# Kernel optimization log

Measured on AMD Instinct MI355X. Metric: run time of the kernel, lower is better.

## Reference

```python
import jax, jax.numpy as jnp
import numpy as np

B, T, F, U = 64, 512, 1024, 64


def setup_inputs() -> dict:
    key = jax.random.key(0)
    ks = jax.random.split(key, 6)
    return {
        "x": jax.random.normal(ks[0], (B, T, F), dtype=jnp.float32),
        "kernel": jax.random.normal(ks[1], (F, U), dtype=jnp.float32) * (1.0 / np.sqrt(F)),
        "bias": jax.random.normal(ks[2], (U,), dtype=jnp.float32) * 0.02,
        "chain_kernel": jax.random.normal(ks[3], (U, U), dtype=jnp.float32) * 0.1,
        "left_boundary": jax.random.normal(ks[4], (U,), dtype=jnp.float32) * 0.1,
        "right_boundary": jax.random.normal(ks[5], (U,), dtype=jnp.float32) * 0.1,
    }


def _viterbi_decode(potentials, chain_kernel):
    # potentials: [B, T, U], chain_kernel: [U, U]
    def step(alpha, pot_t):
        # alpha: [B, U] best score ending in each tag at t-1
        scores = alpha[:, :, None] + chain_kernel[None, :, :] + pot_t[:, None, :]  # [B, U_prev, U_cur]
        return jnp.max(scores, axis=1), jnp.argmax(scores, axis=1)

    pots_t = jnp.moveaxis(potentials[:, 1:], 1, 0)  # [T-1, B, U]
    alpha_last, backptrs = jax.lax.scan(step, potentials[:, 0], pots_t)
    last_tag = jnp.argmax(alpha_last, axis=-1)  # [B]

    def back(tag, bp):
        prev = jnp.take_along_axis(bp, tag[:, None], axis=1)[:, 0]
        return prev, prev

    _, tags = jax.lax.scan(back, last_tag, backptrs, reverse=True)  # [T-1, B], positions 0..T-2
    path = jnp.concatenate([jnp.moveaxis(tags, 0, 1), last_tag[:, None]], axis=1)
    return path.astype(jnp.int32)


def reference(x, kernel, bias, chain_kernel, left_boundary, right_boundary):
    # dense projection (activation = linear)
    potentials = jnp.einsum("btf,fu->btu", x, kernel) + bias  # [B, T, U]
    # boundary energies (mask=None path: add to first/last timestep)
    potentials = potentials.at[:, 0, :].add(left_boundary)
    potentials = potentials.at[:, -1, :].add(right_boundary)
    return _viterbi_decode(potentials, chain_kernel)
```

## Files before the change

### kernel.cpp

```cpp
#include <hip/hip_runtime.h>

#define B_ 64
#define T_ 512
#define F_ 1024
#define U_ 64
#define FK 128
#define NCH (F_ / FK)

__device__ __forceinline__ void block_barrier_lds() {
    asm volatile("s_waitcnt lgkmcnt(0)" ::: "memory");
    __builtin_amdgcn_s_barrier();
    asm volatile("" ::: "memory");
}

__global__ __launch_bounds__(256, 2) void crf_gemm_kernel(
    const float* __restrict__ x, const float* __restrict__ w,
    const float* __restrict__ bias, const float* __restrict__ lb,
    const float* __restrict__ rb, float* __restrict__ pot)
{
    __shared__ float wlds[FK * U_];

    const int tid = threadIdx.x;
    const int rt = tid >> 4;
    const int ut = tid & 15;
    const int n0 = blockIdx.x * 64;
    const int r0 = rt * 4;
    const int u0 = ut * 4;

    float acc[4][4];
#pragma unroll
    for (int i = 0; i < 4; ++i)
#pragma unroll
        for (int j = 0; j < 4; ++j) acc[i][j] = 0.f;

    const float* xrow = x + (size_t)(n0 + r0) * F_;

    float4 wst[8];
#pragma unroll
    for (int l = 0; l < 8; ++l)
        wst[l] = *reinterpret_cast<const float4*>(w + (size_t)(l * 256 + tid) * 4);
#pragma unroll
    for (int l = 0; l < 8; ++l)
        *reinterpret_cast<float4*>(&wlds[(l * 256 + tid) * 4]) = wst[l];
    __syncthreads();

    float4 xp0[4], xp1[4];
#pragma unroll
    for (int i = 0; i < 4; ++i)
        xp0[i] = *reinterpret_cast<const float4*>(xrow + (size_t)i * F_ + 0);
#pragma unroll
    for (int i = 0; i < 4; ++i)
        xp1[i] = *reinterpret_cast<const float4*>(xrow + (size_t)i * F_ + 4);

    for (int c = 0; c < NCH; ++c) {
        if (c + 1 < NCH) {
#pragma unroll
            for (int l = 0; l < 8; ++l)
                wst[l] = *reinterpret_cast<const float4*>(
                    w + (size_t)(c + 1) * (FK * U_) + (size_t)(l * 256 + tid) * 4);
        }

        float4 wc[4];
#pragma unroll
        for (int j = 0; j < 4; ++j)
            wc[j] = *reinterpret_cast<const float4*>(&wlds[(0 + j) * U_ + u0]);

        for (int kk = 0; kk < FK / 4; ++kk) {
            const int kg = (c * FK + kk * 4 + 8) & (F_ - 1);
            float4 xn[4];
#pragma unroll
            for (int i = 0; i < 4; ++i)
                xn[i] = *reinterpret_cast<const float4*>(xrow + (size_t)i * F_ + kg);

            float4 wn[4];
            const int krn = (kk * 4 + 4) & (FK - 1);
#pragma unroll
            for (int j = 0; j < 4; ++j)
                wn[j] = *reinterpret_cast<const float4*>(&wlds[(krn + j) * U_ + u0]);

#pragma unroll
            for (int ff = 0; ff < 4; ++ff) {
                const float4 wf = wc[ff];
#pragma unroll
                for (int i = 0; i < 4; ++i) {
                    const float xs = (ff == 0) ? xp0[i].x : (ff == 1) ? xp0[i].y
                                   : (ff == 2) ? xp0[i].z : xp0[i].w;
                    acc[i][0] = fmaf(xs, wf.x, acc[i][0]);
                    acc[i][1] = fmaf(xs, wf.y, acc[i][1]);
                    acc[i][2] = fmaf(xs, wf.z, acc[i][2]);
                    acc[i][3] = fmaf(xs, wf.w, acc[i][3]);
                }
            }
#pragma unroll
            for (int i = 0; i < 4; ++i) { xp0[i] = xp1[i]; xp1[i] = xn[i]; }
#pragma unroll
            for (int j = 0; j < 4; ++j) wc[j] = wn[j];
        }

        if (c + 1 < NCH) {
            __syncthreads();
#pragma unroll
            for (int l = 0; l < 8; ++l)
                *reinterpret_cast<float4*>(&wlds[(l * 256 + tid) * 4]) = wst[l];
            __syncthreads();
        }
    }

    const int t0 = n0 & (T_ - 1);
    const float4 bs4 = *reinterpret_cast<const float4*>(bias + u0);
    const float4 lb4 = *reinterpret_cast<const float4*>(lb + u0);
    const float4 rb4 = *reinterpret_cast<const float4*>(rb + u0);

#pragma unroll
    for (int i = 0; i < 4; ++i) {
        const int n = n0 + r0 + i;
        const int t = t0 + r0 + i;
        float4 o;
        o.x = acc[i][0] + bs4.x;
        o.y = acc[i][1] + bs4.y;
        o.z = acc[i][2] + bs4.z;
        o.w = acc[i][3] + bs4.w;
        if (t == 0)      { o.x += lb4.x; o.y += lb4.y; o.z += lb4.z; o.w += lb4.w; }
        if (t == T_ - 1) { o.x += rb4.x; o.y += rb4.y; o.z += rb4.z; o.w += rb4.w; }
        *reinterpret_cast<float4*>(pot + (size_t)n * U_ + u0) = o;
    }
}

__global__ __launch_bounds__(256) void crf_viterbi_kernel(
    const float* __restrict__ pot, const float* __restrict__ chain,
    int* __restrict__ path)
{
    const int b = blockIdx.x;
    const int tid = threadIdx.x;
    const int u = tid & 63;
    const int g = tid >> 6;

    __shared__ __align__(16) float alpha_s[64];
    __shared__ float pval[4][64];
    __shared__ int   pidx[4][64];
    __shared__ unsigned char bp[T_ - 1][64];
    __shared__ unsigned char cmap[4][64];
    __shared__ int es[4];

    float chain_r[16];
#pragma unroll
    for (int k = 0; k < 16; ++k)
        chain_r[k] = chain[(size_t)(g * 16 + k) * U_ + u];

    const float* potb = pot + (size_t)b * T_ * U_;

    if (g == 0) alpha_s[u] = potb[u];

    float p0 = potb[1 * U_ + u];
    float p1 = potb[2 * U_ + u];
    float p2 = potb[3 * U_ + u];
    block_barrier_lds();

    for (int t = 1; t < T_; ++t) {
        const int tp = (t + 3 < T_) ? (t + 3) : (T_ - 1);
        const float pnew = potb[(size_t)tp * U_ + u];
        const float pc = p0;

        const float4* a4 = reinterpret_cast<const float4*>(alpha_s);
        float s[16];
#pragma unroll
        for (int q = 0; q < 4; ++q) {
            const float4 av = a4[g * 4 + q];
            s[q * 4 + 0] = (av.x + chain_r[q * 4 + 0]) + pc;
            s[q * 4 + 1] = (av.y + chain_r[q * 4 + 1]) + pc;
            s[q * 4 + 2] = (av.z + chain_r[q * 4 + 2]) + pc;
            s[q * 4 + 3] = (av.w + chain_r[q * 4 + 3]) + pc;
        }
        float tv[8]; int ti[8];
#pragma unroll
        for (int i = 0; i < 8; ++i) {
            const bool gt = s[2 * i + 1] > s[2 * i];
            tv[i] = gt ? s[2 * i + 1] : s[2 * i];
            ti[i] = gt ? 2 * i + 1 : 2 * i;
        }
        float uv[4]; int ui[4];
#pragma unroll
        for (int i = 0; i < 4; ++i) {
            const bool gt = tv[2 * i + 1] > tv[2 * i];
            uv[i] = gt ? tv[2 * i + 1] : tv[2 * i];
            ui[i] = gt ? ti[2 * i + 1] : ti[2 * i];
        }
        const bool g0_ = uv[1] > uv[0];
        const float w0 = g0_ ? uv[1] : uv[0];
        const int   i0 = g0_ ? ui[1] : ui[0];
        const bool g1_ = uv[3] > uv[2];
        const float w1 = g1_ ? uv[3] : uv[2];
        const int   i1 = g1_ ? ui[3] : ui[2];
        const bool gf = w1 > w0;
        const float bv16 = gf ? w1 : w0;
        const int   bi16 = gf ? i1 : i0;

        pval[g][u] = bv16;
        pidx[g][u] = g * 16 + bi16;
        block_barrier_lds();

        if (g == 0) {
            float bv = pval[0][u];
            int   bi = pidx[0][u];
#pragma unroll
            for (int j = 1; j < 4; ++j) {
                const float vv = pval[j][u];
                if (vv > bv) { bv = vv; bi = pidx[j][u]; }
            }
            alpha_s[u] = bv;
            bp[t - 1][u] = (unsigned char)bi;
        }
        block_barrier_lds();

        p0 = p1; p1 = p2; p2 = pnew;
    }

    const int r0c = g * 128;
    const int r1c = (g == 3) ? (T_ - 1) : (g + 1) * 128;

    {
        int tag = u;
        for (int r = r1c - 1; r >= r0c; --r) tag = bp[r][tag];
        cmap[g][u] = (unsigned char)tag;
    }
    block_barrier_lds();

    if (tid == 0) {
        float bvv = alpha_s[0];
        int bii = 0;
        for (int v = 1; v < 64; ++v) {
            const float a = alpha_s[v];
            if (a > bvv) { bvv = a; bii = v; }
        }
        path[(size_t)b * T_ + (T_ - 1)] = bii;
        const int e3 = bii;
        const int e2 = cmap[3][e3];
        const int e1 = cmap[2][e2];
        const int e0 = cmap[1][e1];
        es[0] = e0; es[1] = e1; es[2] = e2; es[3] = e3;
    }
    block_barrier_lds();

    if (u == 0) {
        int tag = es[g];
        int* pb = path + (size_t)b * T_;
        for (int r = r1c - 1; r >= r0c; --r) {
            tag = bp[r][tag];
            pb[r] = tag;
        }
    }
}

extern "C" void kernel_launch(void* const* d_in, const int* in_sizes, int n_in,
                              void* d_out, int out_size, void* d_ws, size_t ws_size,
                              hipStream_t stream) {
    const float* x  = (const float*)d_in[0];
    const float* w  = (const float*)d_in[1];
    const float* bs = (const float*)d_in[2];
    const float* ck = (const float*)d_in[3];
    const float* lb = (const float*)d_in[4];
    const float* rb = (const float*)d_in[5];

    float* pot = (float*)d_ws;
    int* path  = (int*)d_out;

    crf_gemm_kernel<<<dim3(B_ * T_ / 64), dim3(256), 0, stream>>>(x, w, bs, lb, rb, pot);
    crf_viterbi_kernel<<<dim3(B_), dim3(256), 0, stream>>>(pot, ck, path);
}
```

Measured before the change: 413.9 us.

## Run Viterbi recursion in a single wavefront to drop block barriers

The Viterbi kernel moves from four waves per batch (each reducing 16 previous tags, then combining through LDS with two block barriers per step) to one 64-lane wave that reduces all 64 previous tags in registers. Block barriers become wave-level LDS fences, so each timestep avoids cross-wave synchronisation and the partial-result LDS round trip. Backtracking is simplified to every lane chasing pointers from its own tag, with only the winning lane writing the path. In exchange each thread does four times the compare work per step and keeps 64 chain values in registers, and the backtrack is now a single serial chain over all timesteps instead of four chunks in parallel.

```diff
diff --git a/kernel.cpp b/kernel.cpp
--- a/kernel.cpp
+++ b/kernel.cpp
@@ -7,10 +7,9 @@
 #define FK 128
 #define NCH (F_ / FK)
 
-__device__ __forceinline__ void block_barrier_lds() {
+__device__ __forceinline__ void wave_lds_fence() {
     asm volatile("s_waitcnt lgkmcnt(0)" ::: "memory");
-    __builtin_amdgcn_s_barrier();
-    asm volatile("" ::: "memory");
+    __builtin_amdgcn_wave_barrier();
 }
 
 __global__ __launch_bounds__(256, 2) void crf_gemm_kernel(
@@ -126,35 +125,29 @@
     }
 }
 
-__global__ __launch_bounds__(256) void crf_viterbi_kernel(
+__global__ __launch_bounds__(64) void crf_viterbi_kernel(
     const float* __restrict__ pot, const float* __restrict__ chain,
     int* __restrict__ path)
 {
     const int b = blockIdx.x;
-    const int tid = threadIdx.x;
-    const int u = tid & 63;
-    const int g = tid >> 6;
+    const int u = threadIdx.x;
 
     __shared__ __align__(16) float alpha_s[64];
-    __shared__ float pval[4][64];
-    __shared__ int   pidx[4][64];
     __shared__ unsigned char bp[T_ - 1][64];
-    __shared__ unsigned char cmap[4][64];
-    __shared__ int es[4];
-
-    float chain_r[16];
-#pragma unroll
-    for (int k = 0; k < 16; ++k)
-        chain_r[k] = chain[(size_t)(g * 16 + k) * U_ + u];
+
+    float chain_r[64];
+#pragma unroll
+    for (int v = 0; v < 64; ++v)
+        chain_r[v] = chain[(size_t)v * U_ + u];
 
     const float* potb = pot + (size_t)b * T_ * U_;
 
-    if (g == 0) alpha_s[u] = potb[u];
+    alpha_s[u] = potb[u];
 
     float p0 = potb[1 * U_ + u];
     float p1 = potb[2 * U_ + u];
     float p2 = potb[3 * U_ + u];
-    block_barrier_lds();
+    wave_lds_fence();
 
     for (int t = 1; t < T_; ++t) {
         const int tp = (t + 3 < T_) ? (t + 3) : (T_ - 1);
@@ -162,92 +155,69 @@
         const float pc = p0;
 
         const float4* a4 = reinterpret_cast<const float4*>(alpha_s);
-        float s[16];
-#pragma unroll
-        for (int q = 0; q < 4; ++q) {
-            const float4 av = a4[g * 4 + q];
-            s[q * 4 + 0] = (av.x + chain_r[q * 4 + 0]) + pc;
-            s[q * 4 + 1] = (av.y + chain_r[q * 4 + 1]) + pc;
-            s[q * 4 + 2] = (av.z + chain_r[q * 4 + 2]) + pc;
-            s[q * 4 + 3] = (av.w + chain_r[q * 4 + 3]) + pc;
-        }
-        float tv[8]; int ti[8];
+
+        float qv[16]; int qi[16];
+#pragma unroll
+        for (int q = 0; q < 16; ++q) {
+            const float4 av = a4[q];
+            const float s0 = (av.x + chain_r[4 * q + 0]) + pc;
+            const float s1 = (av.y + chain_r[4 * q + 1]) + pc;
+            const float s2 = (av.z + chain_r[4 * q + 2]) + pc;
+            const float s3 = (av.w + chain_r[4 * q + 3]) + pc;
+            const bool ga = s1 > s0;
+            const float m01 = ga ? s1 : s0;
+            const int   i01 = ga ? 4 * q + 1 : 4 * q + 0;
+            const bool gb = s3 > s2;
+            const float m23 = gb ? s3 : s2;
+            const int   i23 = gb ? 4 * q + 3 : 4 * q + 2;
+            const bool gc = m23 > m01;
+            qv[q] = gc ? m23 : m01;
+            qi[q] = gc ? i23 : i01;
+        }
+        float lv[8]; int li[8];
 #pragma unroll
         for (int i = 0; i < 8; ++i) {
-            const bool gt = s[2 * i + 1] > s[2 * i];
-            tv[i] = gt ? s[2 * i + 1] : s[2 * i];
-            ti[i] = gt ? 2 * i + 1 : 2 * i;
-        }
-        float uv[4]; int ui[4];
+            const bool gt = qv[2 * i + 1] > qv[2 * i];
+            lv[i] = gt ? qv[2 * i + 1] : qv[2 * i];
+            li[i] = gt ? qi[2 * i + 1] : qi[2 * i];
+        }
+        float mv[4]; int mi[4];
 #pragma unroll
         for (int i = 0; i < 4; ++i) {
-            const bool gt = tv[2 * i + 1] > tv[2 * i];
-            uv[i] = gt ? tv[2 * i + 1] : tv[2 * i];
-            ui[i] = gt ? ti[2 * i + 1] : ti[2 * i];
-        }
-        const bool g0_ = uv[1] > uv[0];
-        const float w0 = g0_ ? uv[1] : uv[0];
-        const int   i0 = g0_ ? ui[1] : ui[0];
-        const bool g1_ = uv[3] > uv[2];
-        const float w1 = g1_ ? uv[3] : uv[2];
-        const int   i1 = g1_ ? ui[3] : ui[2];
-        const bool gf = w1 > w0;
-        const float bv16 = gf ? w1 : w0;
-        const int   bi16 = gf ? i1 : i0;
-
-        pval[g][u] = bv16;
-        pidx[g][u] = g * 16 + bi16;
-        block_barrier_lds();
-
-        if (g == 0) {
-            float bv = pval[0][u];
-            int   bi = pidx[0][u];
-#pragma unroll
-            for (int j = 1; j < 4; ++j) {
-                const float vv = pval[j][u];
-                if (vv > bv) { bv = vv; bi = pidx[j][u]; }
-            }
-            alpha_s[u] = bv;
-            bp[t - 1][u] = (unsigned char)bi;
-        }
-        block_barrier_lds();
+            const bool gt = lv[2 * i + 1] > lv[2 * i];
+            mv[i] = gt ? lv[2 * i + 1] : lv[2 * i];
+            mi[i] = gt ? li[2 * i + 1] : li[2 * i];
+        }
+        const bool gA = mv[1] > mv[0];
+        const float vA = gA ? mv[1] : mv[0];
+        const int   iA = gA ? mi[1] : mi[0];
+        const bool gB = mv[3] > mv[2];
+        const float vB = gB ? mv[3] : mv[2];
+        const int   iB = gB ? mi[3] : mi[2];
+        const bool gF = vB > vA;
+        const float bv = gF ? vB : vA;
+        const int   gi = gF ? iB : iA;
+
+        alpha_s[u] = bv;
+        bp[t - 1][u] = (unsigned char)gi;
+        wave_lds_fence();
 
         p0 = p1; p1 = p2; p2 = pnew;
     }
 
-    const int r0c = g * 128;
-    const int r1c = (g == 3) ? (T_ - 1) : (g + 1) * 128;
-
-    {
-        int tag = u;
-        for (int r = r1c - 1; r >= r0c; --r) tag = bp[r][tag];
-        cmap[g][u] = (unsigned char)tag;
-    }
-    block_barrier_lds();
-
-    if (tid == 0) {
-        float bvv = alpha_s[0];
-        int bii = 0;
-        for (int v = 1; v < 64; ++v) {
-            const float a = alpha_s[v];
-            if (a > bvv) { bvv = a; bii = v; }
-        }
-        path[(size_t)b * T_ + (T_ - 1)] = bii;
-        const int e3 = bii;
-        const int e2 = cmap[3][e3];
-        const int e1 = cmap[2][e2];
-        const int e0 = cmap[1][e1];
-        es[0] = e0; es[1] = e1; es[2] = e2; es[3] = e3;
-    }
-    block_barrier_lds();
-
-    if (u == 0) {
-        int tag = es[g];
-        int* pb = path + (size_t)b * T_;
-        for (int r = r1c - 1; r >= r0c; --r) {
-            tag = bp[r][tag];
-            pb[r] = tag;
-        }
+    float bvv = alpha_s[0];
+    int win = 0;
+    for (int v = 1; v < 64; ++v) {
+        const float a = alpha_s[v];
+        if (a > bvv) { bvv = a; win = v; }
+    }
+    int* pb = path + (size_t)b * T_;
+    if (u == 0) pb[T_ - 1] = win;
+
+    int tag = u;
+    for (int r = T_ - 2; r >= 0; --r) {
+        tag = bp[r][tag];
+        if (u == win) pb[r] = tag;
     }
 }
 
@@ -265,5 +235,5 @@
     int* path  = (int*)d_out;
 
     crf_gemm_kernel<<<dim3(B_ * T_ / 64), dim3(256), 0, stream>>>(x, w, bs, lb, rb, pot);
-    crf_viterbi_kernel<<<dim3(B_), dim3(256), 0, stream>>>(pot, ck, path);
-}
+    crf_viterbi_kernel<<<dim3(B_), dim3(64), 0, stream>>>(pot, ck, path);
+}
```

New measurement: 763.3 us. 1.84x slower.
